# Performance work log

Measured on AMD Instinct MI355X. Metric: run time of the kernel, lower is better.

Reference implementation:

```python
import jax, jax.numpy as jnp
import numpy as np

N = 50000       # nodes
E = 1600000     # edges (before self-loops)
DIN = 128       # input_dim
HID = 32        # hidden_dim per head
H = 4           # num_heads
HD = HID * H    # 128, concat-head width
DOUT = 128      # output_dim
NC = 2          # num_classes
G = 256         # graphs in batch
NEG_SLOPE = 0.2
BN_EPS = 1e-5


def setup_inputs() -> dict:
    key = jax.random.key(0)
    ks = jax.random.split(key, 20)
    p = lambda k, shp: (jax.random.normal(k, shp, jnp.float32) * 0.05)
    x = jax.random.normal(ks[0], (N, DIN), jnp.float32)
    edge_index = jax.random.randint(ks[1], (2, E), 0, N, dtype=jnp.int32)
    batch = jnp.sort(jax.random.randint(ks[2], (N,), 0, G, dtype=jnp.int32))
    return {
        "x": x, "edge_index": edge_index, "batch": batch,
        # GATConv 1: lin weight [DIN, H*HID], att vectors [H, HID], bias [H*HID]
        "W1": p(ks[3], (DIN, HD)), "a1_src": p(ks[4], (H, HID)), "a1_dst": p(ks[5], (H, HID)), "b1": p(ks[6], (HD,)),
        "bn1_g": jnp.ones((HD,), jnp.float32), "bn1_b": jnp.zeros((HD,), jnp.float32),
        # GATConv 2: in = H*HID
        "W2": p(ks[7], (HD, HD)), "a2_src": p(ks[8], (H, HID)), "a2_dst": p(ks[9], (H, HID)), "b2": p(ks[10], (HD,)),
        "bn2_g": jnp.ones((HD,), jnp.float32), "bn2_b": jnp.zeros((HD,), jnp.float32),
        "L1W": p(ks[11], (HD, DOUT)), "L1b": p(ks[12], (DOUT,)),
        "L2W": p(ks[13], (DOUT, NC)), "L2b": p(ks[14], (NC,)),
    }


def _add_self_loops(edge_index, n):
    loops = jnp.arange(n, dtype=edge_index.dtype)
    return jnp.concatenate([edge_index, jnp.stack([loops, loops])], axis=1)


def _gat_conv(x, edge_index, W, a_src, a_dst, bias):
    # PyG GATConv: h = x @ W -> [N,H,F]; per-edge score = LeakyReLU(a_src.h_src + a_dst.h_dst);
    # softmax over incoming edges of each dst node; weighted scatter-add; concat heads + bias.
    n = x.shape[0]
    h = (x @ W).reshape(n, H, HID)
    src, dst = edge_index[0], edge_index[1]
    alpha_s = jnp.sum(h * a_src[None], axis=-1)   # [N,H]
    alpha_d = jnp.sum(h * a_dst[None], axis=-1)   # [N,H]
    e = jax.nn.leaky_relu(alpha_s[src] + alpha_d[dst], NEG_SLOPE)  # [E,H]
    m = jax.ops.segment_max(e, dst, num_segments=n)                # stable softmax over neighbors
    ex = jnp.exp(e - m[dst])
    s = jax.ops.segment_sum(ex, dst, num_segments=n)
    alpha = ex / (s[dst] + 1e-16)                                  # [E,H]
    out = jax.ops.segment_sum(h[src] * alpha[:, :, None], dst, num_segments=n)  # [N,H,F]
    return out.reshape(n, H * HID) + bias


def _batch_norm(x, gamma, beta):
    mu = jnp.mean(x, axis=0)
    var = jnp.mean((x - mu) ** 2, axis=0)
    return gamma * (x - mu) * jax.lax.rsqrt(var + BN_EPS) + beta


def reference(x, edge_index, batch, W1, a1_src, a1_dst, b1, bn1_g, bn1_b,
              W2, a2_src, a2_dst, b2, bn2_g, bn2_b, L1W, L1b, L2W, L2b):
    ei = _add_self_loops(edge_index, x.shape[0])
    h = jax.nn.relu(_gat_conv(x, ei, W1, a1_src, a1_dst, b1))
    h = _batch_norm(h, bn1_g, bn1_b)
    h = jax.nn.relu(_gat_conv(h, ei, W2, a2_src, a2_dst, b2))
    h = _batch_norm(h, bn2_g, bn2_b)
    # global mean pool over graph ids
    sums = jax.ops.segment_sum(h, batch, num_segments=G)
    cnts = jax.ops.segment_sum(jnp.ones((h.shape[0],), h.dtype), batch, num_segments=G)
    pooled = sums / jnp.maximum(cnts, 1.0)[:, None]   # [G, HD]
    z = jax.nn.relu(pooled @ L1W + L1b)               # dropout inactive at eval
    return z @ L2W + L2b                              # [G, NC]
```

## Files before the change

### kernel.cpp

```cpp
#include <hip/hip_runtime.h>
#include <math.h>

#define NN 50000
#define EE 1600000
#define GG 256
#define PAD 80
#define NB 256
#define EPB 6250
#define NR 8
#define RNG 6250
#define BCAP 960
#define NSH 16

constexpr float NEG = 0.2f;
constexpr float BN_EPS = 1e-5f;

typedef __attribute__((ext_vector_type(8))) short short8;
typedef __attribute__((ext_vector_type(4))) float f32x4;
typedef __attribute__((ext_vector_type(2))) float f32x2;

constexpr int PB_W1 = 0, PB_A1S = 16384, PB_A1D = 16512, PB_B1 = 16640,
              PB_G1 = 16768, PB_BE1 = 16896, PB_W2 = 17024, PB_A2S = 33408,
              PB_A2D = 33536, PB_B2 = 33664, PB_G2 = 33792, PB_BE2 = 33920,
              PB_L1W = 34048, PB_L1B = 50432, PB_L2W = 50560, PB_L2B = 50816,
              PB_TOTAL = 50818;

struct PtrPack { const void* p[16]; };

__device__ __forceinline__ float b2f(unsigned short u) {
  unsigned v = ((unsigned)u) << 16;
  float f;
  __builtin_memcpy(&f, &v, 4);
  return f;
}
__device__ __forceinline__ float b2f_lo(unsigned u) {
  unsigned v = u << 16;
  float f;
  __builtin_memcpy(&f, &v, 4);
  return f;
}
__device__ __forceinline__ float b2f_hi(unsigned u) {
  unsigned v = u & 0xffff0000u;
  float f;
  __builtin_memcpy(&f, &v, 4);
  return f;
}
__device__ __forceinline__ unsigned short f2b(float f) {
  unsigned x;
  __builtin_memcpy(&x, &f, 4);
  unsigned r = x + 0x7FFFu + ((x >> 16) & 1u);
  return (unsigned short)(r >> 16);
}

__device__ __forceinline__ void pkfma(f32x2& acc, unsigned u, f32x2 wp) {
  f32x2 p = {b2f_lo(u), b2f_hi(u)};
  asm("v_pk_fma_f32 %0, %1, %2, %0" : "+v"(acc) : "v"(p), "v"(wp));
}

__global__ __launch_bounds__(256) void k_prep(PtrPack pk, const unsigned short* __restrict__ xb,
                                              const int* __restrict__ batch,
                                              const int* __restrict__ esrc,
                                              const int* __restrict__ edst,
                                              int* __restrict__ flag,
                                              float* __restrict__ pb,
                                              int* __restrict__ starts, float* __restrict__ bnacc,
                                              int* __restrict__ ctrs,
                                              unsigned char* __restrict__ hist,
                                              unsigned* __restrict__ buck, int* __restrict__ bcnt,
                                              unsigned short* __restrict__ Wt1,
                                              float* __restrict__ wzero,
                                              float* __restrict__ poolsum) {
  const int segoff[17] = {0, 16384, 16512, 16640, 16768, 16896, 17024, 33408,
                          33536, 33664, 33792, 33920, 34048, 50432, 50560, 50816, 50818};
  __shared__ unsigned hcnt[25000];
  __shared__ int bc[NR];
  __shared__ int cs;
  int c = blockIdx.x, t = threadIdx.x;
  if (t == 0) cs = 0;
  if (t < NR) bc[t] = 0;
  for (int j = t; j < 25000; j += 256) hcnt[j] = 0u;
  __syncthreads();
  int sane = 0;
  for (int i = t; i < 4096; i += 256) {
    float a = fabsf(b2f(xb[i]));
    if (a > 1e-4f && a < 100.f) sane++;
  }
  atomicAdd(&cs, sane);
  int e0 = c * EPB;
  for (int i = t; i < EPB; i += 256) {
    int e = e0 + i;
    int d = edst[e];
    if ((unsigned)d >= (unsigned)NN) continue;
    int s = esrc[e];
    if ((unsigned)s >= (unsigned)NN) s = 0;
    int sh = (d & 1) * 16;
    unsigned old = atomicAdd(&hcnt[d >> 1], 1u << sh);
    unsigned rank = (old >> sh) & 0xFFFFu;
    if (rank > 7u) continue;
    int r = d / RNG;
    int dl = d - r * RNG;
    int pos = atomicAdd(&bc[r], 1);
    if (pos < BCAP)
      buck[(c * NR + r) * BCAP + pos] = ((unsigned)s << 16) | ((unsigned)dl << 3) | rank;
  }
  __syncthreads();
  int bf = (cs > 3482) ? 1 : 0;
  if (c == 0 && t == 0) *flag = bf;
  if (t < NR) bcnt[c * NR + t] = min(bc[t], BCAP);
  for (int j = t; j < NN; j += 256) {
    unsigned cc = (hcnt[j >> 1] >> ((j & 1) * 16)) & 0xFFFFu;
    hist[c * NN + j] = (unsigned char)min(cc, 255u);
  }
  for (int j = t; j < 199; j += 256) {
    int i = c * 199 + j;
    if (i < PB_TOTAL) {
      int seg = 0;
      while (i >= segoff[seg + 1]) seg++;
      int k = i - segoff[seg];
      pb[i] = bf ? b2f(((const unsigned short*)pk.p[seg])[k]) : ((const float*)pk.p[seg])[k];
    }
  }
  for (int j = t; j < 64; j += 256) {
    int i = c * 64 + j;
    int n = i & 127, k = i >> 7;
    Wt1[n * 128 + k] = bf ? ((const unsigned short*)pk.p[0])[k * 128 + n]
                          : f2b(((const float*)pk.p[0])[k * 128 + n]);
  }
  for (int j = t; j < 128; j += 256) poolsum[c * 128 + j] = 0.f;
  if (t < 32) bnacc[c * 32 + t] = 0.f;
  for (int j = t; j < 196; j += 256) {
    int n = c * 196 + j;
    if (n < NN) {
      int bb = batch[n];
      bb = min(max(bb, 0), GG - 1);
      int bp = (n == 0) ? -1 : batch[n - 1];
      bp = min(max(bp, -1), GG - 1);
      for (int gg = bp + 1; gg <= bb; gg++) starts[gg] = n;
      if (n == NN - 1)
        for (int gg = bb + 1; gg <= GG; gg++) starts[gg] = NN;
    }
  }
  if (c == 255 && t < 8) ctrs[t] = 0;
}

__global__ __launch_bounds__(256) void k_base(const unsigned char* __restrict__ hist,
                                              unsigned char* __restrict__ base,
                                              int* __restrict__ cnt) {
  int d = blockIdx.x * 256 + threadIdx.x;
  if (d >= NN) return;
  int run = 0;
  for (int b = 0; b < NB; b++) {
    int h = hist[b * NN + d];
    base[b * NN + d] = (unsigned char)min(run, 255);
    run += h;
  }
  cnt[d] = run;
}

__device__ __forceinline__ void gemm_body(float* cst, int bid,
                                          const unsigned short* __restrict__ Xb,
                                          const float* __restrict__ Xf, int bfm,
                                          const unsigned short* __restrict__ Wt,
                                          const float* __restrict__ shiftW,
                                          const float* __restrict__ aS,
                                          const float* __restrict__ aD,
                                          unsigned short* __restrict__ Y,
                                          float* __restrict__ as_, float* __restrict__ ad_) {
  int t = threadIdx.x;
  int row0 = bid * 64;
  int w = t >> 6, lane = t & 63;
  int m = lane & 15, quad = lane >> 4;
  int rA = min(row0 + w * 16 + m, NN - 1);
  short8 a4[4];
  if (bfm) {
    const short8* xp = (const short8*)(Xb + rA * 128);
#pragma unroll
    for (int kk = 0; kk < 4; kk++) a4[kk] = xp[kk * 4 + quad];
  } else {
#pragma unroll
    for (int kk = 0; kk < 4; kk++) {
      const float* xf = Xf + rA * 128 + kk * 32 + quad * 8;
#pragma unroll
      for (int j = 0; j < 8; j++) a4[kk][j] = (short)f2b(xf[j]);
    }
  }
  f32x4 acc[8] = {};
#pragma unroll
  for (int kk = 0; kk < 4; kk++) {
    int ko = kk * 32 + quad * 8;
#pragma unroll
    for (int n0 = 0; n0 < 8; n0++) {
      short8 b = *(const short8*)(Wt + (n0 * 16 + m) * 128 + ko);
      acc[n0] = __builtin_amdgcn_mfma_f32_16x16x32_bf16(a4[kk], b, acc[n0], 0, 0, 0);
    }
  }
#pragma unroll
  for (int n0 = 0; n0 < 8; n0++)
#pragma unroll
    for (int r = 0; r < 4; r++)
      cst[(w * 16 + quad * 4 + r) * 130 + n0 * 16 + m] = acc[n0][r];
  __syncthreads();
  int cg = t & 31, rg = t >> 5;
  int c0 = cg * 4;
  float a_s[4], a_d[4], sw[4];
#pragma unroll
  for (int j = 0; j < 4; j++) {
    a_s[j] = aS[c0 + j];
    a_d[j] = aD[c0 + j];
    sw[j] = shiftW[c0 + j];
  }
#pragma unroll
  for (int i = 0; i < 8; i++) {
    int rl = rg + i * 8;
    int row = row0 + rl;
    float v0 = cst[rl * 130 + c0 + 0] + sw[0];
    float v1 = cst[rl * 130 + c0 + 1] + sw[1];
    float v2 = cst[rl * 130 + c0 + 2] + sw[2];
    float v3 = cst[rl * 130 + c0 + 3] + sw[3];
    if (row < NN) {
      uint2 pk2;
      pk2.x = (unsigned)f2b(v0) | ((unsigned)f2b(v1) << 16);
      pk2.y = (unsigned)f2b(v2) | ((unsigned)f2b(v3) << 16);
      *reinterpret_cast<uint2*>(&Y[row * 128 + c0]) = pk2;
    }
    float ps = v0 * a_s[0] + v1 * a_s[1] + v2 * a_s[2] + v3 * a_s[3];
    float pd = v0 * a_d[0] + v1 * a_d[1] + v2 * a_d[2] + v3 * a_d[3];
    ps += __shfl_xor(ps, 1); ps += __shfl_xor(ps, 2); ps += __shfl_xor(ps, 4);
    pd += __shfl_xor(pd, 1); pd += __shfl_xor(pd, 2); pd += __shfl_xor(pd, 4);
    if ((cg & 7) == 0 && row < NN) {
      int hh = cg >> 3;
      as_[row * 4 + hh] = ps;
      ad_[row * 4 + hh] = pd;
    }
  }
}

__global__ __launch_bounds__(256) void k_fillgemm(const unsigned* __restrict__ buck,
                                                  const int* __restrict__ bcnt,
                                                  const unsigned char* __restrict__ base,
                                                  unsigned short* __restrict__ adj,
                                                  const unsigned short* __restrict__ Xb,
                                                  const float* __restrict__ Xf,
                                                  const int* __restrict__ flagp,
                                                  const unsigned short* __restrict__ Wt,
                                                  const float* __restrict__ shiftW,
                                                  const float* __restrict__ aS,
                                                  const float* __restrict__ aD,
                                                  unsigned short* __restrict__ Y,
                                                  float* __restrict__ as_, float* __restrict__ ad_) {
  __shared__ float cst[64 * 130];
  int idx = blockIdx.x;
  int t = threadIdx.x;
  if (idx < NB) {
    int r = idx & 7, g = idx >> 3;
    int dbase = r * RNG;
#pragma unroll 1
    for (int j = 0; j < 8; j++) {
      int c = g * 8 + j;
      int n = bcnt[c * NR + r];
      const unsigned* bk = buck + (c * NR + r) * BCAP;
      const unsigned char* bs = base + c * NN;
      for (int i = t; i < n; i += 256) {
        unsigned p = bk[i];
        int s = p >> 16;
        int dl = (p >> 3) & 0x1FFF;
        int rank = p & 7;
        int d = dbase + dl;
        int slot = (int)bs[d] + rank;
        if (slot < PAD) adj[d * PAD + slot] = (unsigned short)s;
      }
    }
  } else {
    gemm_body(cst, idx - NB, Xb, Xf, *flagp, Wt, shiftW, aS, aD, Y, as_, ad_);
  }
}

__global__ __launch_bounds__(256) void k_gemm(const unsigned short* __restrict__ Xb,
                                              const unsigned short* __restrict__ Wt,
                                              const float* __restrict__ shiftW,
                                              const float* __restrict__ aS,
                                              const float* __restrict__ aD,
                                              unsigned short* __restrict__ Y,
                                              float* __restrict__ as_, float* __restrict__ ad_) {
  __shared__ float cst[64 * 130];
  gemm_body(cst, blockIdx.x, Xb, nullptr, 1, Wt, shiftW, aS, aD, Y, as_, ad_);
}

__global__ __launch_bounds__(256) void k_agg(const unsigned short* __restrict__ adj,
                                             const int* __restrict__ cnt,
                                             const float4* __restrict__ asrc4,
                                             const float4* __restrict__ adst4,
                                             const uint4* __restrict__ hin4,
                                             const float* __restrict__ bias,
                                             unsigned short* __restrict__ out) {
  __shared__ float wq[4][PAD][4];
  __shared__ int ws[4][PAD];
  int t = threadIdx.x;
  int wid = t >> 6, lane = t & 63;
  int n = blockIdx.x * 4 + wid;
  int deg = cnt[n];
  if (deg < 0) deg = 0;
  if (deg > PAD - 1) deg = PAD - 1;
  int tot = deg + 1;
  int beg = n * PAD;
  float4 ad4 = adst4[n];
  float ls0 = 0.f, ls1 = 0.f, ls2 = 0.f, ls3 = 0.f;
  for (int b = lane; b < tot; b += 64) {
    int s = (b < deg) ? (int)adj[beg + b] : n;
    if ((unsigned)s >= (unsigned)NN) s = n;
    float4 a = asrc4[s];
    float s0 = a.x + ad4.x; s0 = s0 > 0.f ? s0 : NEG * s0;
    float s1 = a.y + ad4.y; s1 = s1 > 0.f ? s1 : NEG * s1;
    float s2 = a.z + ad4.z; s2 = s2 > 0.f ? s2 : NEG * s2;
    float s3 = a.w + ad4.w; s3 = s3 > 0.f ? s3 : NEG * s3;
    float e0 = __expf(s0), e1 = __expf(s1), e2 = __expf(s2), e3 = __expf(s3);
    ls0 += e0; ls1 += e1; ls2 += e2; ls3 += e3;
    *reinterpret_cast<float4*>(&wq[wid][b][0]) = make_float4(e0, e1, e2, e3);
    ws[wid][b] = s;
  }
  asm volatile("" ::: "memory");
  __builtin_amdgcn_wave_barrier();
  int g = lane >> 4, L = lane & 15, hd = L >> 2;
  const float (*wrow)[4] = wq[wid];
  const int* srow = ws[wid];
  f32x2 acc2[4] = {};
  int e = g;
  for (; e + 12 < tot; e += 16) {
    float w1 = wrow[e][hd], w2 = wrow[e + 4][hd], w3 = wrow[e + 8][hd], w4 = wrow[e + 12][hd];
    int s1 = srow[e], s2 = srow[e + 4], s3 = srow[e + 8], s4 = srow[e + 12];
    uint4 v1 = hin4[s1 * 16 + L];
    uint4 v2 = hin4[s2 * 16 + L];
    uint4 v3 = hin4[s3 * 16 + L];
    uint4 v4 = hin4[s4 * 16 + L];
    f32x2 p1 = {w1, w1}, p2 = {w2, w2}, p3 = {w3, w3}, p4 = {w4, w4};
    pkfma(acc2[0], v1.x, p1); pkfma(acc2[1], v1.y, p1);
    pkfma(acc2[2], v1.z, p1); pkfma(acc2[3], v1.w, p1);
    pkfma(acc2[0], v2.x, p2); pkfma(acc2[1], v2.y, p2);
    pkfma(acc2[2], v2.z, p2); pkfma(acc2[3], v2.w, p2);
    pkfma(acc2[0], v3.x, p3); pkfma(acc2[1], v3.y, p3);
    pkfma(acc2[2], v3.z, p3); pkfma(acc2[3], v3.w, p3);
    pkfma(acc2[0], v4.x, p4); pkfma(acc2[1], v4.y, p4);
    pkfma(acc2[2], v4.z, p4); pkfma(acc2[3], v4.w, p4);
  }
  for (; e < tot; e += 4) {
    float wv = wrow[e][hd];
    int s = srow[e];
    uint4 v = hin4[s * 16 + L];
    f32x2 p = {wv, wv};
    pkfma(acc2[0], v.x, p); pkfma(acc2[1], v.y, p);
    pkfma(acc2[2], v.z, p); pkfma(acc2[3], v.w, p);
  }
#pragma unroll
  for (int j = 0; j < 4; j++) {
    acc2[j].x += __shfl_xor(acc2[j].x, 16);
    acc2[j].y += __shfl_xor(acc2[j].y, 16);
    acc2[j].x += __shfl_xor(acc2[j].x, 32);
    acc2[j].y += __shfl_xor(acc2[j].y, 32);
  }
#pragma unroll
  for (int mm = 1; mm < 64; mm <<= 1) {
    ls0 += __shfl_xor(ls0, mm);
    ls1 += __shfl_xor(ls1, mm);
    ls2 += __shfl_xor(ls2, mm);
    ls3 += __shfl_xor(ls3, mm);
  }
  if (g == 0) {
    float den = (hd == 0) ? ls0 : (hd == 1) ? ls1 : (hd == 2) ? ls2 : ls3;
    float inv = 1.0f / (den + 1e-16f);
    const float4* bp = reinterpret_cast<const float4*>(bias + L * 8);
    float4 b0 = bp[0], b1 = bp[1];
    float o0 = acc2[0].x * inv + b0.x;
    float o1 = acc2[0].y * inv + b0.y;
    float o2 = acc2[1].x * inv + b0.z;
    float o3 = acc2[1].y * inv + b0.w;
    float o4 = acc2[2].x * inv + b1.x;
    float o5 = acc2[2].y * inv + b1.y;
    float o6 = acc2[3].x * inv + b1.z;
    float o7 = acc2[3].y * inv + b1.w;
    o0 = o0 > 0.f ? o0 : 0.f;
    o1 = o1 > 0.f ? o1 : 0.f;
    o2 = o2 > 0.f ? o2 : 0.f;
    o3 = o3 > 0.f ? o3 : 0.f;
    o4 = o4 > 0.f ? o4 : 0.f;
    o5 = o5 > 0.f ? o5 : 0.f;
    o6 = o6 > 0.f ? o6 : 0.f;
    o7 = o7 > 0.f ? o7 : 0.f;
    uint4 pk4;
    pk4.x = (unsigned)f2b(o0) | ((unsigned)f2b(o1) << 16);
    pk4.y = (unsigned)f2b(o2) | ((unsigned)f2b(o3) << 16);
    pk4.z = (unsigned)f2b(o4) | ((unsigned)f2b(o5) << 16);
    pk4.w = (unsigned)f2b(o6) | ((unsigned)f2b(o7) << 16);
    *reinterpret_cast<uint4*>(&out[n * 128 + L * 8]) = pk4;
  }
}

__global__ __launch_bounds__(128) void k_bnstats(const unsigned* __restrict__ x32,
                                                 float* __restrict__ accum, int* __restrict__ ctr,
                                                 const float* __restrict__ g, const float* __restrict__ b,
                                                 float* __restrict__ scale, float* __restrict__ shift,
                                                 const float* __restrict__ W2f, float* __restrict__ sw2,
                                                 unsigned short* __restrict__ Wt2,
                                                 const int* __restrict__ batch,
                                                 float* __restrict__ poolsum) {
  __shared__ int lastflag;
  __shared__ float shs[128];
  __shared__ float scs[128];
  int t = threadIdx.x;
  int c2 = t & 63, half = t >> 6;
  int sh = blockIdx.x & (NSH - 1);
  int r0 = blockIdx.x * 196;
  int r1 = min(r0 + 196, NN);
  float s0 = 0.f, q0 = 0.f, s1 = 0.f, q1 = 0.f;
  if (poolsum) {
    int curg = -1;
    float p0 = 0.f, p1 = 0.f;
    for (int r = r0 + half; r < r1; r += 2) {
      int gg = batch[r];
      gg = min(max(gg, 0), GG - 1);
      if (gg != curg) {
        if (curg >= 0) {
          atomicAdd(&poolsum[curg * 128 + 2 * c2], p0);
          atomicAdd(&poolsum[curg * 128 + 2 * c2 + 1], p1);
        }
        curg = gg; p0 = 0.f; p1 = 0.f;
      }
      unsigned v = x32[r * 64 + c2];
      float lo = b2f_lo(v), hi = b2f_hi(v);
      s0 += lo; q0 += lo * lo; p0 += lo;
      s1 += hi; q1 += hi * hi; p1 += hi;
    }
    if (curg >= 0) {
      atomicAdd(&poolsum[curg * 128 + 2 * c2], p0);
      atomicAdd(&poolsum[curg * 128 + 2 * c2 + 1], p1);
    }
  } else {
    for (int r = r0 + half; r < r1; r += 2) {
      unsigned v = x32[r * 64 + c2];
      float lo = b2f_lo(v), hi = b2f_hi(v);
      s0 += lo; q0 += lo * lo;
      s1 += hi; q1 += hi * hi;
    }
  }
  float* ac = accum + sh * 256;
  atomicAdd(&ac[2 * c2], s0);
  atomicAdd(&ac[2 * c2 + 1], s1);
  atomicAdd(&ac[128 + 2 * c2], q0);
  atomicAdd(&ac[128 + 2 * c2 + 1], q1);
  __threadfence();
  if (t == 0) {
    int done = atomicAdd(ctr, 1);
    lastflag = (done == (int)gridDim.x - 1) ? 1 : 0;
  }
  __syncthreads();
  if (lastflag) {
    float ss = 0.f, qq = 0.f;
#pragma unroll
    for (int s2 = 0; s2 < NSH; s2++) {
      ss += atomicAdd(&accum[s2 * 256 + t], 0.f);
      qq += atomicAdd(&accum[s2 * 256 + 128 + t], 0.f);
    }
    float inv = 1.0f / NN;
    float mu = ss * inv;
    float var = qq * inv - mu * mu;
    float rs = rsqrtf(var + BN_EPS);
    float sc = g[t] * rs;
    float shv = b[t] - mu * sc;
    scale[t] = sc;
    shift[t] = shv;
    shs[t] = shv;
    scs[t] = sc;
    __syncthreads();
    if (W2f) {
      float s = 0.f;
      for (int k = 0; k < 128; k++) s += shs[k] * W2f[k * 128 + t];
      sw2[t] = s;
      for (int i = t; i < 16384; i += 128) {
        int n = i & 127, k = i >> 7;
        Wt2[n * 128 + k] = f2b(scs[k] * W2f[k * 128 + n]);
      }
    }
  }
}

__global__ __launch_bounds__(128) void k_head(const float* __restrict__ poolsum,
                                              const int* __restrict__ starts,
                                              const float* __restrict__ scale, const float* __restrict__ shift,
                                              const float* __restrict__ L1W, const float* __restrict__ L1b,
                                              const float* __restrict__ L2W, const float* __restrict__ L2b,
                                              const int* __restrict__ flagp, void* __restrict__ outp) {
  int g = blockIdx.x, t = threadIdx.x;
  int b0 = starts[g], b1 = starts[g + 1];
  b0 = min(max(b0, 0), NN);
  b1 = min(max(b1, 0), NN);
  int cnt = b1 - b0;
  __shared__ float pooled[128];
  float s = poolsum[g * 128 + t];
  pooled[t] = (cnt > 0) ? (s / cnt) * scale[t] + shift[t] : 0.f;
  __syncthreads();
  float z = L1b[t];
  for (int k = 0; k < 128; k++) z += pooled[k] * L1W[k * 128 + t];
  z = z > 0.f ? z : 0.f;
  __shared__ float r0a[128], r1a[128];
  r0a[t] = z * L2W[t * 2 + 0];
  r1a[t] = z * L2W[t * 2 + 1];
  __syncthreads();
  for (int d = 64; d >= 1; d >>= 1) {
    if (t < d) {
      r0a[t] += r0a[t + d];
      r1a[t] += r1a[t + d];
    }
    __syncthreads();
  }
  if (t == 0) {
    float o0 = r0a[0] + L2b[0];
    float o1 = r1a[0] + L2b[1];
    if (*flagp) {
      unsigned short* ob = (unsigned short*)outp;
      ob[g * 2 + 0] = f2b(o0);
      ob[g * 2 + 1] = f2b(o1);
    } else {
      float* of = (float*)outp;
      of[g * 2 + 0] = o0;
      of[g * 2 + 1] = o1;
    }
  }
}

extern "C" void kernel_launch(void* const* d_in, const int* in_sizes, int n_in,
                              void* d_out, int out_size, void* d_ws, size_t ws_size,
                              hipStream_t stream) {
  (void)in_sizes; (void)n_in; (void)out_size; (void)ws_size;
  const int* ei = (const int*)d_in[1];
  const int* batch = (const int*)d_in[2];

  float* ws = (float*)d_ws;
  size_t o = 0;
  int* flag = (int*)(ws + o);   o += 16;
  int* ctrs = (int*)(ws + o);   o += 16;
  float* pb = ws + o;           o += 51200;
  float* bnacc = ws + o;        o += 8192;
  float* scale1 = ws + o;       o += 128;
  float* shift1 = ws + o;       o += 128;
  float* scale2 = ws + o;       o += 128;
  float* shift2 = ws + o;       o += 128;
  float* wzero = ws + o;        o += 128;
  float* sw2 = ws + o;          o += 128;
  unsigned short* Wt1 = (unsigned short*)(ws + o); o += 8192;
  unsigned short* Wt2 = (unsigned short*)(ws + o); o += 8192;
  float* poolsum = ws + o;      o += GG * 128;
  int* cnt = (int*)(ws + o);    o += 50016;
  int* starts = (int*)(ws + o); o += 512;
  int* bcnt = (int*)(ws + o);   o += 2048;
  float* asrc = ws + o;         o += 200000;
  float* adst = ws + o;         o += 200000;
  unsigned* buck = (unsigned*)(ws + o);            o += NB * NR * BCAP;
  unsigned short* adj = (unsigned short*)(ws + o); o += NN * PAD / 2;
  unsigned short* hA = (unsigned short*)(ws + o);  o += 3200000;
  unsigned short* hB = (unsigned short*)(ws + o);  o += 3200000;

  unsigned char* hist = (unsigned char*)hB;
  unsigned char* base = (unsigned char*)hA;

  const int* esrc = ei;
  const int* edst = ei + EE;

  PtrPack pk;
  for (int i = 0; i < 16; i++) pk.p[i] = d_in[3 + i];

  k_prep<<<NB, 256, 0, stream>>>(pk, (const unsigned short*)d_in[0], batch, esrc, edst,
                                 flag, pb, starts, bnacc, ctrs, hist, buck, bcnt,
                                 Wt1, wzero, poolsum);
  k_base<<<196, 256, 0, stream>>>(hist, base, cnt);

  k_fillgemm<<<NB + 782, 256, 0, stream>>>(buck, bcnt, base, adj,
                                           (const unsigned short*)d_in[0], (const float*)d_in[0],
                                           flag, Wt1, wzero,
                                           pb + PB_A1S, pb + PB_A1D, hB, asrc, adst);
  k_agg<<<NN / 4, 256, 0, stream>>>(adj, cnt, (const float4*)asrc, (const float4*)adst,
                                    (const uint4*)hB, pb + PB_B1, hA);
  k_bnstats<<<256, 128, 0, stream>>>((const unsigned*)hA, bnacc, ctrs + 1,
                                     pb + PB_G1, pb + PB_BE1, scale1, shift1,
                                     pb + PB_W2, sw2, Wt2, nullptr, nullptr);

  k_gemm<<<782, 256, 0, stream>>>(hA, Wt2, sw2, pb + PB_A2S, pb + PB_A2D, hB, asrc, adst);
  k_agg<<<NN / 4, 256, 0, stream>>>(adj, cnt, (const float4*)asrc, (const float4*)adst,
                                    (const uint4*)hB, pb + PB_B2, hA);
  k_bnstats<<<256, 128, 0, stream>>>((const unsigned*)hA, bnacc + 4096, ctrs + 2,
                                     pb + PB_G2, pb + PB_BE2, scale2, shift2,
                                     nullptr, nullptr, nullptr, batch, poolsum);

  k_head<<<GG, 128, 0, stream>>>(poolsum, starts, scale2, shift2,
                                 pb + PB_L1W, pb + PB_L1B,
                                 pb + PB_L2W, pb + PB_L2B, flag, d_out);
}
```

Baseline: 408.7 us.

## Partition aggregation edges into contiguous per-group chunks and widen prep blocks

```diff
diff --git a/kernel.cpp b/kernel.cpp
--- a/kernel.cpp
+++ b/kernel.cpp
@@ -57,7 +57,7 @@
   asm("v_pk_fma_f32 %0, %1, %2, %0" : "+v"(acc) : "v"(p), "v"(wp));
 }
 
-__global__ __launch_bounds__(256) void k_prep(PtrPack pk, const unsigned short* __restrict__ xb,
+__global__ __launch_bounds__(512) void k_prep(PtrPack pk, const unsigned short* __restrict__ xb,
                                               const int* __restrict__ batch,
                                               const int* __restrict__ esrc,
                                               const int* __restrict__ edst,
@@ -78,16 +78,16 @@
   int c = blockIdx.x, t = threadIdx.x;
   if (t == 0) cs = 0;
   if (t < NR) bc[t] = 0;
-  for (int j = t; j < 25000; j += 256) hcnt[j] = 0u;
+  for (int j = t; j < 25000; j += 512) hcnt[j] = 0u;
   __syncthreads();
   int sane = 0;
-  for (int i = t; i < 4096; i += 256) {
+  for (int i = t; i < 4096; i += 512) {
     float a = fabsf(b2f(xb[i]));
     if (a > 1e-4f && a < 100.f) sane++;
   }
   atomicAdd(&cs, sane);
   int e0 = c * EPB;
-  for (int i = t; i < EPB; i += 256) {
+  for (int i = t; i < EPB; i += 512) {
     int e = e0 + i;
     int d = edst[e];
     if ((unsigned)d >= (unsigned)NN) continue;
@@ -107,11 +107,11 @@
   int bf = (cs > 3482) ? 1 : 0;
   if (c == 0 && t == 0) *flag = bf;
   if (t < NR) bcnt[c * NR + t] = min(bc[t], BCAP);
-  for (int j = t; j < NN; j += 256) {
+  for (int j = t; j < NN; j += 512) {
     unsigned cc = (hcnt[j >> 1] >> ((j & 1) * 16)) & 0xFFFFu;
     hist[c * NN + j] = (unsigned char)min(cc, 255u);
   }
-  for (int j = t; j < 199; j += 256) {
+  for (int j = t; j < 199; j += 512) {
     int i = c * 199 + j;
     if (i < PB_TOTAL) {
       int seg = 0;
@@ -120,15 +120,15 @@
       pb[i] = bf ? b2f(((const unsigned short*)pk.p[seg])[k]) : ((const float*)pk.p[seg])[k];
     }
   }
-  for (int j = t; j < 64; j += 256) {
+  for (int j = t; j < 64; j += 512) {
     int i = c * 64 + j;
     int n = i & 127, k = i >> 7;
     Wt1[n * 128 + k] = bf ? ((const unsigned short*)pk.p[0])[k * 128 + n]
                           : f2b(((const float*)pk.p[0])[k * 128 + n]);
   }
-  for (int j = t; j < 128; j += 256) poolsum[c * 128 + j] = 0.f;
+  for (int j = t; j < 128; j += 512) poolsum[c * 128 + j] = 0.f;
   if (t < 32) bnacc[c * 32 + t] = 0.f;
-  for (int j = t; j < 196; j += 256) {
+  for (int j = t; j < 196; j += 512) {
     int n = c * 196 + j;
     if (n < NN) {
       int bb = batch[n];
@@ -293,8 +293,8 @@
                                              const uint4* __restrict__ hin4,
                                              const float* __restrict__ bias,
                                              unsigned short* __restrict__ out) {
-  __shared__ float wq[4][PAD][4];
-  __shared__ int ws[4][PAD];
+  __shared__ float wq2[4][4][PAD];
+  __shared__ unsigned soffs[4][PAD];
   int t = threadIdx.x;
   int wid = t >> 6, lane = t & 63;
   int n = blockIdx.x * 4 + wid;
@@ -302,37 +302,48 @@
   if (deg < 0) deg = 0;
   if (deg > PAD - 1) deg = PAD - 1;
   int tot = deg + 1;
+  int W = (((tot + 3) >> 2) + 3) & ~3;
+  int WL = 4 * W;
   int beg = n * PAD;
   float4 ad4 = adst4[n];
   float ls0 = 0.f, ls1 = 0.f, ls2 = 0.f, ls3 = 0.f;
-  for (int b = lane; b < tot; b += 64) {
-    int s = (b < deg) ? (int)adj[beg + b] : n;
-    if ((unsigned)s >= (unsigned)NN) s = n;
-    float4 a = asrc4[s];
-    float s0 = a.x + ad4.x; s0 = s0 > 0.f ? s0 : NEG * s0;
-    float s1 = a.y + ad4.y; s1 = s1 > 0.f ? s1 : NEG * s1;
-    float s2 = a.z + ad4.z; s2 = s2 > 0.f ? s2 : NEG * s2;
-    float s3 = a.w + ad4.w; s3 = s3 > 0.f ? s3 : NEG * s3;
-    float e0 = __expf(s0), e1 = __expf(s1), e2 = __expf(s2), e3 = __expf(s3);
-    ls0 += e0; ls1 += e1; ls2 += e2; ls3 += e3;
-    *reinterpret_cast<float4*>(&wq[wid][b][0]) = make_float4(e0, e1, e2, e3);
-    ws[wid][b] = s;
+  for (int b = lane; b < WL; b += 64) {
+    if (b < tot) {
+      int s = (b < deg) ? (int)adj[beg + b] : n;
+      if ((unsigned)s >= (unsigned)NN) s = n;
+      float4 a = asrc4[s];
+      float s0 = a.x + ad4.x; s0 = s0 > 0.f ? s0 : NEG * s0;
+      float s1 = a.y + ad4.y; s1 = s1 > 0.f ? s1 : NEG * s1;
+      float s2 = a.z + ad4.z; s2 = s2 > 0.f ? s2 : NEG * s2;
+      float s3 = a.w + ad4.w; s3 = s3 > 0.f ? s3 : NEG * s3;
+      float e0 = __expf(s0), e1 = __expf(s1), e2 = __expf(s2), e3 = __expf(s3);
+      ls0 += e0; ls1 += e1; ls2 += e2; ls3 += e3;
+      wq2[wid][0][b] = e0; wq2[wid][1][b] = e1;
+      wq2[wid][2][b] = e2; wq2[wid][3][b] = e3;
+      soffs[wid][b] = (unsigned)s * 256u;
+    } else {
+      wq2[wid][0][b] = 0.f; wq2[wid][1][b] = 0.f;
+      wq2[wid][2][b] = 0.f; wq2[wid][3][b] = 0.f;
+      soffs[wid][b] = (unsigned)n * 256u;
+    }
   }
   asm volatile("" ::: "memory");
   __builtin_amdgcn_wave_barrier();
   int g = lane >> 4, L = lane & 15, hd = L >> 2;
-  const float (*wrow)[4] = wq[wid];
-  const int* srow = ws[wid];
+  const char* hb = (const char*)hin4;
+  unsigned Loff = (unsigned)L * 16u;
+  const float* wrow = &wq2[wid][hd][0];
+  const unsigned* srow = &soffs[wid][0];
   f32x2 acc2[4] = {};
-  int e = g;
-  for (; e + 12 < tot; e += 16) {
-    float w1 = wrow[e][hd], w2 = wrow[e + 4][hd], w3 = wrow[e + 8][hd], w4 = wrow[e + 12][hd];
-    int s1 = srow[e], s2 = srow[e + 4], s3 = srow[e + 8], s4 = srow[e + 12];
-    uint4 v1 = hin4[s1 * 16 + L];
-    uint4 v2 = hin4[s2 * 16 + L];
-    uint4 v3 = hin4[s3 * 16 + L];
-    uint4 v4 = hin4[s4 * 16 + L];
-    f32x2 p1 = {w1, w1}, p2 = {w2, w2}, p3 = {w3, w3}, p4 = {w4, w4};
+  int e0w = g * W, e1w = e0w + W;
+  for (int e = e0w; e < e1w; e += 4) {
+    f32x4 w4 = *(const f32x4*)(wrow + e);
+    uint4 o4 = *(const uint4*)(srow + e);
+    uint4 v1 = *(const uint4*)(hb + (o4.x + Loff));
+    uint4 v2 = *(const uint4*)(hb + (o4.y + Loff));
+    uint4 v3 = *(const uint4*)(hb + (o4.z + Loff));
+    uint4 v4 = *(const uint4*)(hb + (o4.w + Loff));
+    f32x2 p1 = {w4.x, w4.x}, p2 = {w4.y, w4.y}, p3 = {w4.z, w4.z}, p4 = {w4.w, w4.w};
     pkfma(acc2[0], v1.x, p1); pkfma(acc2[1], v1.y, p1);
     pkfma(acc2[2], v1.z, p1); pkfma(acc2[3], v1.w, p1);
     pkfma(acc2[0], v2.x, p2); pkfma(acc2[1], v2.y, p2);
@@ -341,14 +352,6 @@
     pkfma(acc2[2], v3.z, p3); pkfma(acc2[3], v3.w, p3);
     pkfma(acc2[0], v4.x, p4); pkfma(acc2[1], v4.y, p4);
     pkfma(acc2[2], v4.z, p4); pkfma(acc2[3], v4.w, p4);
-  }
-  for (; e < tot; e += 4) {
-    float wv = wrow[e][hd];
-    int s = srow[e];
-    uint4 v = hin4[s * 16 + L];
-    f32x2 p = {wv, wv};
-    pkfma(acc2[0], v.x, p); pkfma(acc2[1], v.y, p);
-    pkfma(acc2[2], v.z, p); pkfma(acc2[3], v.w, p);
   }
 #pragma unroll
   for (int j = 0; j < 4; j++) {
@@ -567,7 +570,7 @@
   PtrPack pk;
   for (int i = 0; i < 16; i++) pk.p[i] = d_in[3 + i];
 
-  k_prep<<<NB, 256, 0, stream>>>(pk, (const unsigned short*)d_in[0], batch, esrc, edst,
+  k_prep<<<NB, 512, 0, stream>>>(pk, (const unsigned short*)d_in[0], batch, esrc, edst,
                                  flag, pb, starts, bnacc, ctrs, hist, buck, bcnt,
                                  Wt1, wzero, poolsum);
   k_base<<<196, 256, 0, stream>>>(hist, base, cnt);
```

Measured after the change: 392.4 us. 4.0% less time.
